# Optimization experiments

Measured on AMD Instinct MI355X. Metric: run time of the kernel, lower is better.

The kernel has to match this reference:

```python
import jax, jax.numpy as jnp
import numpy as np

B, T, D, H = 2, 2048, 768, 12
HS = D // H           # head_size = 64
FF = 4 * D            # feed_forward_multiplier = 4 -> hidden 3072
HALF = FF // 2        # SwiGLU halves hidden -> 1536
EPS = 1e-8


def rmsnorm(x, scale):
    # RMSNorm with p=-1: full-dim L2 norm / sqrt(d), then x/(rms+eps)*scale
    d = x.shape[-1]
    rms = jnp.linalg.norm(x, axis=-1, keepdims=True) * (d ** -0.5)
    return scale * (x / (rms + EPS))


def setup_inputs() -> dict:
    key = jax.random.key(0)
    ks = jax.random.split(key, 12)
    s = 0.02
    return {
        "x":  jax.random.normal(ks[0], (B, T, D), dtype=jnp.float32),
        "Wq": jax.random.normal(ks[1], (H, D, HS), dtype=jnp.float32) * s,
        "Wk": jax.random.normal(ks[2], (H, D, HS), dtype=jnp.float32) * s,
        "Wv": jax.random.normal(ks[3], (H, D, HS), dtype=jnp.float32) * s,
        "Wo": jax.random.normal(ks[4], (D, D), dtype=jnp.float32) * s,
        "bo": jnp.zeros((D,), dtype=jnp.float32),
        "W1": jax.random.normal(ks[5], (D, FF), dtype=jnp.float32) * s,
        "b1": jnp.zeros((FF,), dtype=jnp.float32),
        "W2": jax.random.normal(ks[6], (HALF, D), dtype=jnp.float32) * s,
        "b2": jnp.zeros((D,), dtype=jnp.float32),
        "g1": jnp.ones((D,), dtype=jnp.float32),
        "g2": jnp.ones((D,), dtype=jnp.float32),
    }


def reference(x, Wq, Wk, Wv, Wo, bo, W1, b1, W2, b2, g1, g2):
    Bx, Tx, Dx = x.shape
    # --- Multi-head causal attention (pre-RMSNorm, residual) ---
    h = rmsnorm(x, g1)
    q = jnp.einsum('btd,hdk->bhtk', h, Wq)
    k = jnp.einsum('btd,hdk->bhtk', h, Wk)
    v = jnp.einsum('btd,hdk->bhtk', h, Wv)
    # NOTE: original scales by C**-0.5 where C = embed_dim (not head_size)
    scores = jnp.einsum('bhtk,bhsk->bhts', q, k) * (Dx ** -0.5)
    causal = jnp.tril(jnp.ones((Tx, Tx), dtype=bool))
    scores = jnp.where(causal, scores, -jnp.inf)
    wei = jax.nn.softmax(scores, axis=-1)
    attn = jnp.einsum('bhts,bhsk->bhtk', wei, v)
    attn = attn.transpose(0, 2, 1, 3).reshape(Bx, Tx, Dx)  # concat heads
    x = x + attn @ Wo + bo
    # --- SwiGLU FFN (pre-RMSNorm, residual) ---
    h2 = rmsnorm(x, g2)
    u = h2 @ W1 + b1
    a, gate = jnp.split(u, 2, axis=-1)  # chunk: first half = value, second = gate
    x = x + (jax.nn.silu(gate) * a) @ W2 + b2
    return x
```

## Files before the change

### kernel.cpp

```cpp
#include <hip/hip_runtime.h>
#include <math.h>

#define TDIM 2048
#define DDIM 768
#define NH   12
#define NROWS 4096
#define EPSV 1e-8f
#define SCALE 0.03608439182435161f

typedef __bf16 bf16_t;
typedef bf16_t bf16x8 __attribute__((ext_vector_type(8)));
typedef bf16_t bf16x4 __attribute__((ext_vector_type(4)));
typedef bf16_t bf16x2 __attribute__((ext_vector_type(2)));
typedef float  floatx4 __attribute__((ext_vector_type(4)));

__device__ __forceinline__ void glds16(const bf16_t* g, bf16_t* l) {
    __builtin_amdgcn_global_load_lds(
        (const __attribute__((address_space(1))) void*)g,
        (__attribute__((address_space(3))) void*)l, 16, 0, 0);
}

__global__ __launch_bounds__(256) void pack_all(
    const float* __restrict__ Wq, const float* __restrict__ Wk,
    const float* __restrict__ Wv, const float* __restrict__ Wo,
    const float* __restrict__ W1, const float* __restrict__ W2,
    bf16_t* __restrict__ qkvw, bf16_t* __restrict__ wo,
    bf16_t* __restrict__ w1, bf16_t* __restrict__ w2)
{
    int bid = blockIdx.x;
    const float* src; bf16_t* dst;
    int srcld, dstld, k0, n0;
    int remap = 0;
    if (bid < 144) {
        int kx = bid % 12, nx = bid / 12;
        src = Wo; dst = wo; srcld = 768; dstld = 768; k0 = kx * 64; n0 = nx * 64;
    } else if (bid < 720) {
        int t = bid - 144; int kx = t % 12, nx = t / 12;
        src = W1; dst = w1; srcld = 3072; dstld = 768; k0 = kx * 64; n0 = nx * 64;
        remap = 1;
    } else if (bid < 1008) {
        int t = bid - 720; int kx = t % 24, nx = t / 24;
        src = W2; dst = w2; srcld = 768; dstld = 1536; k0 = kx * 64; n0 = nx * 64;
    } else {
        int t = bid - 1008; int kx = t % 12, y = t / 12;
        int sel = y / 12, h = y - sel * 12;
        src = ((sel == 0) ? Wq : (sel == 1) ? Wk : Wv) + (size_t)h * 768 * 64;
        dst = qkvw + (size_t)(sel * 768 + h * 64) * 768;
        srcld = 64; dstld = 768; k0 = kx * 64; n0 = 0;
    }
    __shared__ float Ts[64][65];
    int tid = threadIdx.x;
    int r = tid >> 2, c = (tid & 3) * 16;
    const float* s = src + (size_t)(k0 + r) * srcld + n0 + c;
    #pragma unroll
    for (int i = 0; i < 4; i++) {
        float4 t = *(const float4*)(s + i * 4);
        Ts[r][c + i*4 + 0] = t.x; Ts[r][c + i*4 + 1] = t.y;
        Ts[r][c + i*4 + 2] = t.z; Ts[r][c + i*4 + 3] = t.w;
    }
    __syncthreads();
    int n = tid >> 2, kk = (tid & 3) * 16;
    bf16x8 o0, o1;
    #pragma unroll
    for (int i = 0; i < 8; i++) {
        o0[i] = (bf16_t)Ts[kk + i][n];
        o1[i] = (bf16_t)Ts[kk + 8 + i][n];
    }
    int oc = n0 + n;
    if (remap) oc = (oc < 1536) ? (oc * 2) : ((oc - 1536) * 2 + 1);
    bf16_t* d = dst + (size_t)oc * dstld + k0 + kk;
    *(bf16x8*)d = o0;
    *(bf16x8*)(d + 8) = o1;
}

__global__ __launch_bounds__(256) void rmsnorm_bf(
    const float* __restrict__ x, const float* __restrict__ g,
    bf16_t* __restrict__ out)
{
    int row = blockIdx.x;
    int tid = threadIdx.x;
    const float* xr = x + (size_t)row * DDIM;
    float v0 = xr[tid], v1 = xr[tid + 256], v2 = xr[tid + 512];
    float s = v0*v0 + v1*v1 + v2*v2;
    #pragma unroll
    for (int off = 32; off > 0; off >>= 1)
        s += __shfl_down(s, off, 64);
    __shared__ float red[4];
    __shared__ float tot;
    if ((tid & 63) == 0) red[tid >> 6] = s;
    __syncthreads();
    if (tid == 0) tot = red[0] + red[1] + red[2] + red[3];
    __syncthreads();
    float rms = sqrtf(tot * (1.0f / DDIM));
    float inv = 1.0f / (rms + EPSV);
    bf16_t* orow = out + (size_t)row * DDIM;
    orow[tid]       = (bf16_t)(g[tid]       * v0 * inv);
    orow[tid + 256] = (bf16_t)(g[tid + 256] * v1 * inv);
    orow[tid + 512] = (bf16_t)(g[tid + 512] * v2 * inv);
}

template<int TM, int EPI>
__global__ __launch_bounds__(256) void gemm_bf16(
    const bf16_t* __restrict__ A, const bf16_t* __restrict__ BT, int K,
    float* __restrict__ Cf, bf16_t* __restrict__ Cb, int ldc,
    const float* __restrict__ bias, const float* __restrict__ resid)
{
    constexpr int MT = TM / 32;
    __shared__ bf16_t As0[TM][32], As1[TM][32];
    __shared__ bf16_t Bs0[128][32], Bs1[128][32];
    int tid = threadIdx.x;
    int wave = tid >> 6, lane = tid & 63;
    int lrow = lane & 15, quad = lane >> 4;
    int wm = wave >> 1, wn = wave & 1;

    int m0 = blockIdx.y * TM;
    int n0 = blockIdx.x * 128;

    int srow = lane >> 2, scol = (lane & 3) * 8;
    const bf16_t* Ag = A  + ((size_t)m0 + wave * (TM/4) + srow) * K + scol;
    const bf16_t* Bg = BT + ((size_t)n0 + wave * 32 + srow) * K + scol;

    floatx4 acc[MT][4];
    #pragma unroll
    for (int mt = 0; mt < MT; mt++)
        #pragma unroll
        for (int nt = 0; nt < 4; nt++)
            #pragma unroll
            for (int r = 0; r < 4; r++) acc[mt][nt][r] = 0.f;

    for (int k0 = 0; k0 < K; k0 += 64) {
        __syncthreads();
        #pragma unroll
        for (int i = 0; i < TM/64; i++) {
            glds16(Ag + (size_t)(i*16) * K + k0,      &As0[wave*(TM/4) + i*16][0]);
            glds16(Ag + (size_t)(i*16) * K + k0 + 32, &As1[wave*(TM/4) + i*16][0]);
        }
        #pragma unroll
        for (int i = 0; i < 2; i++) {
            glds16(Bg + (size_t)(i*16) * K + k0,      &Bs0[wave*32 + i*16][0]);
            glds16(Bg + (size_t)(i*16) * K + k0 + 32, &Bs1[wave*32 + i*16][0]);
        }
        __syncthreads();

        bf16x8 af0[MT], af1[MT], bf0[4], bf1[4];
        #pragma unroll
        for (int mt = 0; mt < MT; mt++) {
            af0[mt] = *(const bf16x8*)&As0[wm*(TM/2) + mt*16 + lrow][quad * 8];
            af1[mt] = *(const bf16x8*)&As1[wm*(TM/2) + mt*16 + lrow][quad * 8];
        }
        #pragma unroll
        for (int nt = 0; nt < 4; nt++) {
            bf0[nt] = *(const bf16x8*)&Bs0[wn*64 + nt*16 + lrow][quad * 8];
            bf1[nt] = *(const bf16x8*)&Bs1[wn*64 + nt*16 + lrow][quad * 8];
        }
        #pragma unroll
        for (int mt = 0; mt < MT; mt++)
            #pragma unroll
            for (int nt = 0; nt < 4; nt++) {
                acc[mt][nt] = __builtin_amdgcn_mfma_f32_16x16x32_bf16(
                    bf0[nt], af0[mt], acc[mt][nt], 0, 0, 0);
                acc[mt][nt] = __builtin_amdgcn_mfma_f32_16x16x32_bf16(
                    bf1[nt], af1[mt], acc[mt][nt], 0, 0, 0);
            }
    }

    int crow0 = m0 + wm * (TM/2);
    int ccol0 = n0 + wn * 64;
    #pragma unroll
    for (int mt = 0; mt < MT; mt++) {
        int row = crow0 + mt * 16 + lrow;
        #pragma unroll
        for (int nt = 0; nt < 4; nt++) {
            int col = ccol0 + nt * 16 + quad * 4;
            floatx4 a = acc[mt][nt];
            if constexpr (EPI == 1) {
                int c = col >> 1;
                float2 ba = *(const float2*)(bias + c);
                float2 bg = *(const float2*)(bias + 1536 + c);
                float a0 = a[0] + ba.x, g0 = a[1] + bg.x;
                float a1 = a[2] + ba.y, g1 = a[3] + bg.y;
                bf16x2 v;
                v[0] = (bf16_t)(a0 * (g0 / (1.0f + __expf(-g0))));
                v[1] = (bf16_t)(a1 * (g1 / (1.0f + __expf(-g1))));
                *(bf16x2*)(Cb + (size_t)row * ldc + c) = v;
            } else {
                size_t off = (size_t)row * ldc + col;
                float4 bv = make_float4(0.f, 0.f, 0.f, 0.f);
                if (bias) bv = *(const float4*)(bias + col);
                float4 rs = make_float4(0.f, 0.f, 0.f, 0.f);
                if (resid) rs = *(const float4*)(resid + off);
                if (Cf) {
                    float4 v;
                    v.x = a[0] + bv.x + rs.x; v.y = a[1] + bv.y + rs.y;
                    v.z = a[2] + bv.z + rs.z; v.w = a[3] + bv.w + rs.w;
                    *(float4*)(Cf + off) = v;
                } else {
                    bf16x4 v;
                    v[0] = (bf16_t)(a[0] + bv.x + rs.x);
                    v[1] = (bf16_t)(a[1] + bv.y + rs.y);
                    v[2] = (bf16_t)(a[2] + bv.z + rs.z);
                    v[3] = (bf16_t)(a[3] + bv.w + rs.w);
                    *(bf16x4*)(Cb + off) = v;
                }
            }
        }
    }
}

__global__ __launch_bounds__(256) void vt_kernel(
    const bf16_t* __restrict__ qkv, bf16_t* __restrict__ vt)
{
    __shared__ bf16_t Ts[64][72];
    int t0 = blockIdx.x * 64;
    int bh = blockIdx.y;
    int b = bh / NH, h = bh - b * NH;
    int tid = threadIdx.x;
    int r = tid >> 2, c = (tid & 3) * 16;
    const bf16_t* src = qkv + ((size_t)b * TDIM + t0 + r) * 2304 + 1536 + h * 64 + c;
    *(bf16x8*)&Ts[r][c]     = *(const bf16x8*)src;
    *(bf16x8*)&Ts[r][c + 8] = *(const bf16x8*)(src + 8);
    __syncthreads();
    int d = tid >> 2, tt = (tid & 3) * 16;
    bf16x8 o0, o1;
    #pragma unroll
    for (int i = 0; i < 8; i++) {
        o0[i] = Ts[tt + i][d];
        o1[i] = Ts[tt + 8 + i][d];
    }
    bf16_t* dst = vt + ((size_t)bh * 64 + d) * TDIM + t0 + tt;
    *(bf16x8*)dst = o0;
    *(bf16x8*)(dst + 8) = o1;
}

__global__ __launch_bounds__(256) void attn_mfma(
    const bf16_t* __restrict__ qkv, const bf16_t* __restrict__ vt,
    bf16_t* __restrict__ o)
{
    const int QS = 2304;
    int bid = blockIdx.x;
    int c = bid & 255, slot = bid >> 8;
    int x = c & 31, g = c >> 5;
    int qt, bh;
    if (slot == 0)      { bh = g;      qt = x; }
    else if (slot == 1) { bh = 8 + g;  qt = (x + 16) & 31; }
    else                { bh = 16 + g; qt = (x < 16) ? (31 - 2 * x) : (62 - 2 * x); }
    int b = bh / NH, h = bh - b * NH;
    int tid = threadIdx.x;
    int wave = tid >> 6, lane = tid & 63;
    int lrow = lane & 15, quad = lane >> 4;

    __shared__ bf16_t Ks[2][64][72];
    __shared__ bf16_t Vts[2][64][72];
    __shared__ bf16_t Ps[4][16][72];

    size_t rbase = (size_t)b * TDIM;
    int q0 = qt * 64, qrow_w = q0 + wave * 16;

    const bf16_t* qp = qkv + (rbase + qrow_w + lrow) * QS + h * 64;
    bf16x8 qf[2];
    qf[0] = *(const bf16x8*)(qp + quad * 8);
    qf[1] = *(const bf16x8*)(qp + 32 + quad * 8);

    floatx4 o_acc[4];
    #pragma unroll
    for (int mt = 0; mt < 4; mt++)
        #pragma unroll
        for (int r = 0; r < 4; r++) o_acc[mt][r] = 0.f;
    float m_r = -INFINITY, l_r = 0.f;

    int srow = tid >> 2;
    int scol = (tid & 3) * 16;
    const bf16_t* kbase = qkv + (rbase + srow) * QS + 768 + h * 64 + scol;
    const bf16_t* vbase = vt + ((size_t)bh * 64 + srow) * TDIM + scol;

    bf16x8 kr0 = *(const bf16x8*)kbase;
    bf16x8 kr1 = *(const bf16x8*)(kbase + 8);
    bf16x8 vr0 = *(const bf16x8*)vbase;
    bf16x8 vr1 = *(const bf16x8*)(vbase + 8);
    *(bf16x8*)&Ks[0][srow][scol]      = kr0;
    *(bf16x8*)&Ks[0][srow][scol + 8]  = kr1;
    *(bf16x8*)&Vts[0][srow][scol]     = vr0;
    *(bf16x8*)&Vts[0][srow][scol + 8] = vr1;
    if (qt >= 1) {
        const bf16_t* kp = kbase + (size_t)64 * QS;
        const bf16_t* vp = vbase + 64;
        kr0 = *(const bf16x8*)kp;  kr1 = *(const bf16x8*)(kp + 8);
        vr0 = *(const bf16x8*)vp;  vr1 = *(const bf16x8*)(vp + 8);
    }
    asm volatile("s_waitcnt lgkmcnt(0)" ::: "memory");
    __builtin_amdgcn_s_barrier();

    for (int s = 0; s <= qt; s++) {
        int cur = s & 1;

        floatx4 sfrag[4];
        __builtin_amdgcn_s_setprio(1);
        #pragma unroll
        for (int nt = 0; nt < 4; nt++) {
            floatx4 a;
            #pragma unroll
            for (int r = 0; r < 4; r++) a[r] = 0.f;
            #pragma unroll
            for (int kf = 0; kf < 2; kf++) {
                bf16x8 afr = *(const bf16x8*)&Ks[cur][nt * 16 + lrow][kf * 32 + quad * 8];
                a = __builtin_amdgcn_mfma_f32_16x16x32_bf16(afr, qf[kf], a, 0, 0, 0);
            }
            sfrag[nt] = a;
        }
        __builtin_amdgcn_s_setprio(0);

        if (s == qt) {
            int qg = qrow_w + lrow;
            #pragma unroll
            for (int nt = 0; nt < 4; nt++)
                #pragma unroll
                for (int r = 0; r < 4; r++) {
                    int kc = s * 64 + nt * 16 + quad * 4 + r;
                    sfrag[nt][r] = (kc > qg) ? -INFINITY : sfrag[nt][r] * SCALE;
                }
        } else {
            #pragma unroll
            for (int nt = 0; nt < 4; nt++)
                #pragma unroll
                for (int r = 0; r < 4; r++) sfrag[nt][r] *= SCALE;
        }

        float mx = sfrag[0][0];
        #pragma unroll
        for (int nt = 0; nt < 4; nt++)
            #pragma unroll
            for (int r = 0; r < 4; r++) mx = fmaxf(mx, sfrag[nt][r]);
        mx = fmaxf(mx, __shfl_xor(mx, 16, 64));
        mx = fmaxf(mx, __shfl_xor(mx, 32, 64));
        if (__any(mx > m_r + 8.0f)) {
            float mn = fmaxf(m_r, mx);
            float alpha = __expf(m_r - mn);
            m_r = mn;
            l_r *= alpha;
            #pragma unroll
            for (int mt = 0; mt < 4; mt++)
                #pragma unroll
                for (int r = 0; r < 4; r++) o_acc[mt][r] *= alpha;
        }

        float ls = 0.f;
        #pragma unroll
        for (int nt = 0; nt < 4; nt++) {
            bf16x4 pv;
            #pragma unroll
            for (int r = 0; r < 4; r++) {
                float p = __expf(sfrag[nt][r] - m_r);
                ls += p;
                pv[r] = (bf16_t)p;
            }
            *(bf16x4*)&Ps[wave][lrow][nt * 16 + quad * 4] = pv;
        }
        ls += __shfl_xor(ls, 16, 64);
        ls += __shfl_xor(ls, 32, 64);
        l_r += ls;

        __builtin_amdgcn_s_setprio(1);
        #pragma unroll
        for (int kf = 0; kf < 2; kf++) {
            bf16x8 pfr = *(const bf16x8*)&Ps[wave][lrow][kf * 32 + quad * 8];
            #pragma unroll
            for (int mt = 0; mt < 4; mt++) {
                bf16x8 vfr = *(const bf16x8*)&Vts[cur][mt * 16 + lrow][kf * 32 + quad * 8];
                o_acc[mt] = __builtin_amdgcn_mfma_f32_16x16x32_bf16(vfr, pfr, o_acc[mt], 0, 0, 0);
            }
        }
        __builtin_amdgcn_s_setprio(0);

        if (s < qt) {
            int nxt = cur ^ 1;
            *(bf16x8*)&Ks[nxt][srow][scol]      = kr0;
            *(bf16x8*)&Ks[nxt][srow][scol + 8]  = kr1;
            *(bf16x8*)&Vts[nxt][srow][scol]     = vr0;
            *(bf16x8*)&Vts[nxt][srow][scol + 8] = vr1;
        }

        if (s + 2 <= qt) {
            const bf16_t* kp = kbase + (size_t)(s + 2) * 64 * QS;
            const bf16_t* vp = vbase + (size_t)(s + 2) * 64;
            kr0 = *(const bf16x8*)kp;  kr1 = *(const bf16x8*)(kp + 8);
            vr0 = *(const bf16x8*)vp;  vr1 = *(const bf16x8*)(vp + 8);
        }

        asm volatile("s_waitcnt lgkmcnt(0)" ::: "memory");
        __builtin_amdgcn_s_barrier();
    }

    float inv = 1.0f / l_r;
    size_t rb = (rbase + qrow_w + lrow) * DDIM + h * 64;
    #pragma unroll
    for (int mt = 0; mt < 4; mt++) {
        bf16x4 ov;
        #pragma unroll
        for (int r = 0; r < 4; r++) ov[r] = (bf16_t)(o_acc[mt][r] * inv);
        *(bf16x4*)(o + rb + mt * 16 + quad * 4) = ov;
    }
}

extern "C" void kernel_launch(void* const* d_in, const int* in_sizes, int n_in,
                              void* d_out, int out_size, void* d_ws, size_t ws_size,
                              hipStream_t stream) {
    const float* x  = (const float*)d_in[0];
    const float* Wq = (const float*)d_in[1];
    const float* Wk = (const float*)d_in[2];
    const float* Wv = (const float*)d_in[3];
    const float* Wo = (const float*)d_in[4];
    const float* bo = (const float*)d_in[5];
    const float* W1 = (const float*)d_in[6];
    const float* b1 = (const float*)d_in[7];
    const float* W2 = (const float*)d_in[8];
    const float* b2 = (const float*)d_in[9];
    const float* g1 = (const float*)d_in[10];
    const float* g2 = (const float*)d_in[11];
    float* out = (float*)d_out;
    char* ws = (char*)d_ws;

    bf16_t* qkvw_bt = (bf16_t*)(ws);
    bf16_t* wo_bt   = (bf16_t*)(ws + 3538944);
    bf16_t* w1_bt   = (bf16_t*)(ws + 4718592);
    bf16_t* w2_bt   = (bf16_t*)(ws + 9437184);
    bf16_t* h_bf    = (bf16_t*)(ws + 11796480);
    bf16_t* qkv     = (bf16_t*)(ws + 18087936);
    bf16_t* attn_bf = (bf16_t*)(ws + 36962304);
    bf16_t* sw_bf   = (bf16_t*)(ws + 68419584);
    bf16_t* vt      = (bf16_t*)(ws + 81002496);

    pack_all<<<1440, 256, 0, stream>>>(Wq, Wk, Wv, Wo, W1, W2,
                                       qkvw_bt, wo_bt, w1_bt, w2_bt);

    rmsnorm_bf<<<NROWS, 256, 0, stream>>>(x, g1, h_bf);

    gemm_bf16<128, 0><<<dim3(18, 32), 256, 0, stream>>>(
        h_bf, qkvw_bt, 768, nullptr, qkv, 2304, nullptr, nullptr);

    vt_kernel<<<dim3(32, 24), 256, 0, stream>>>(qkv, vt);

    attn_mfma<<<768, 256, 0, stream>>>(qkv, vt, attn_bf);

    gemm_bf16<64, 0><<<dim3(6, 64), 256, 0, stream>>>(
        attn_bf, wo_bt, 768, out, nullptr, 768, bo, x);

    rmsnorm_bf<<<NROWS, 256, 0, stream>>>(out, g2, h_bf);

    gemm_bf16<128, 1><<<dim3(24, 32), 256, 0, stream>>>(
        h_bf, w1_bt, 768, nullptr, sw_bf, 1536, b1, nullptr);

    gemm_bf16<64, 0><<<dim3(6, 64), 256, 0, stream>>>(
        sw_bf, w2_bt, 1536, out, nullptr, 768, b2, out);
}
```

Before: 265.4 us.

## Split attention KV loop across two wave groups with final softmax merge

The attention kernel now launches 512 threads per block. Two groups of four waves each handle alternating KV tiles, each group keeping its own online-softmax state. At the end the partial outputs and max/sum statistics are merged through shared memory. This halves the serial KV-loop length per block and raises parallelism for the causal attention, at the cost of extra block-wide barriers, a merge step, larger register pressure under launch bounds of 512, and more shared memory per block.

```diff
diff --git a/kernel.cpp b/kernel.cpp
--- a/kernel.cpp
+++ b/kernel.cpp
@@ -232,29 +232,33 @@
     *(bf16x8*)(dst + 8) = o1;
 }
 
-__global__ __launch_bounds__(256) void attn_mfma(
+__global__ __launch_bounds__(512) void attn_mfma(
     const bf16_t* __restrict__ qkv, const bf16_t* __restrict__ vt,
     bf16_t* __restrict__ o)
 {
     const int QS = 2304;
     int bid = blockIdx.x;
     int c = bid & 255, slot = bid >> 8;
-    int x = c & 31, g = c >> 5;
+    int x = c & 31, gg = c >> 5;
     int qt, bh;
-    if (slot == 0)      { bh = g;      qt = x; }
-    else if (slot == 1) { bh = 8 + g;  qt = (x + 16) & 31; }
-    else                { bh = 16 + g; qt = (x < 16) ? (31 - 2 * x) : (62 - 2 * x); }
+    if (slot == 0)      { bh = gg;      qt = x; }
+    else if (slot == 1) { bh = 8 + gg;  qt = (x + 16) & 31; }
+    else                { bh = 16 + gg; qt = (x < 16) ? (31 - 2 * x) : (62 - 2 * x); }
     int b = bh / NH, h = bh - b * NH;
     int tid = threadIdx.x;
     int wave = tid >> 6, lane = tid & 63;
+    int ww = wave & 3;
+    int g  = wave >> 2;
     int lrow = lane & 15, quad = lane >> 4;
 
     __shared__ bf16_t Ks[2][64][72];
     __shared__ bf16_t Vts[2][64][72];
-    __shared__ bf16_t Ps[4][16][72];
+    __shared__ char ps_raw[8 * 16 * 72 * 2];
+    __shared__ float Ml[4][16][2];
+    bf16_t (*Ps)[16][72] = (bf16_t (*)[16][72])ps_raw;
 
     size_t rbase = (size_t)b * TDIM;
-    int q0 = qt * 64, qrow_w = q0 + wave * 16;
+    int q0 = qt * 64, qrow_w = q0 + ww * 16;
 
     const bf16_t* qp = qkv + (rbase + qrow_w + lrow) * QS + h * 64;
     bf16x8 qf[2];
@@ -268,136 +272,161 @@
         for (int r = 0; r < 4; r++) o_acc[mt][r] = 0.f;
     float m_r = -INFINITY, l_r = 0.f;
 
-    int srow = tid >> 2;
-    int scol = (tid & 3) * 16;
+    int st = tid & 255;
+    int srow = st >> 2;
+    int scol = (st & 3) * 16;
     const bf16_t* kbase = qkv + (rbase + srow) * QS + 768 + h * 64 + scol;
     const bf16_t* vbase = vt + ((size_t)bh * 64 + srow) * TDIM + scol;
 
-    bf16x8 kr0 = *(const bf16x8*)kbase;
-    bf16x8 kr1 = *(const bf16x8*)(kbase + 8);
-    bf16x8 vr0 = *(const bf16x8*)vbase;
-    bf16x8 vr1 = *(const bf16x8*)(vbase + 8);
-    *(bf16x8*)&Ks[0][srow][scol]      = kr0;
-    *(bf16x8*)&Ks[0][srow][scol + 8]  = kr1;
-    *(bf16x8*)&Vts[0][srow][scol]     = vr0;
-    *(bf16x8*)&Vts[0][srow][scol + 8] = vr1;
-    if (qt >= 1) {
-        const bf16_t* kp = kbase + (size_t)64 * QS;
-        const bf16_t* vp = vbase + 64;
+    bf16x8 kr0, kr1, vr0, vr1;
+    if (g <= qt) {
+        const bf16_t* kp = kbase + (size_t)g * 64 * QS;
+        const bf16_t* vp = vbase + (size_t)g * 64;
         kr0 = *(const bf16x8*)kp;  kr1 = *(const bf16x8*)(kp + 8);
         vr0 = *(const bf16x8*)vp;  vr1 = *(const bf16x8*)(vp + 8);
+        *(bf16x8*)&Ks[g][srow][scol]      = kr0;
+        *(bf16x8*)&Ks[g][srow][scol + 8]  = kr1;
+        *(bf16x8*)&Vts[g][srow][scol]     = vr0;
+        *(bf16x8*)&Vts[g][srow][scol + 8] = vr1;
+    }
+    if (g + 2 <= qt) {
+        const bf16_t* kp = kbase + (size_t)(g + 2) * 64 * QS;
+        const bf16_t* vp = vbase + (size_t)(g + 2) * 64;
+        kr0 = *(const bf16x8*)kp;  kr1 = *(const bf16x8*)(kp + 8);
+        vr0 = *(const bf16x8*)vp;  vr1 = *(const bf16x8*)(vp + 8);
     }
     asm volatile("s_waitcnt lgkmcnt(0)" ::: "memory");
     __builtin_amdgcn_s_barrier();
 
-    for (int s = 0; s <= qt; s++) {
-        int cur = s & 1;
-
-        floatx4 sfrag[4];
-        __builtin_amdgcn_s_setprio(1);
-        #pragma unroll
-        for (int nt = 0; nt < 4; nt++) {
-            floatx4 a;
-            #pragma unroll
-            for (int r = 0; r < 4; r++) a[r] = 0.f;
+    int nit = (qt >> 1) + 1;
+    for (int i = 0; i < nit; i++) {
+        int s = 2 * i + g;
+        if (s <= qt) {
+            floatx4 sfrag[4];
+            __builtin_amdgcn_s_setprio(1);
+            #pragma unroll
+            for (int nt = 0; nt < 4; nt++) {
+                floatx4 a;
+                #pragma unroll
+                for (int r = 0; r < 4; r++) a[r] = 0.f;
+                #pragma unroll
+                for (int kf = 0; kf < 2; kf++) {
+                    bf16x8 afr = *(const bf16x8*)&Ks[g][nt * 16 + lrow][kf * 32 + quad * 8];
+                    a = __builtin_amdgcn_mfma_f32_16x16x32_bf16(afr, qf[kf], a, 0, 0, 0);
+                }
+                sfrag[nt] = a;
+            }
+            __builtin_amdgcn_s_setprio(0);
+
+            if (s == qt) {
+                int qg = qrow_w + lrow;
+                #pragma unroll
+                for (int nt = 0; nt < 4; nt++)
+                    #pragma unroll
+                    for (int r = 0; r < 4; r++) {
+                        int kc = s * 64 + nt * 16 + quad * 4 + r;
+                        sfrag[nt][r] = (kc > qg) ? -INFINITY : sfrag[nt][r] * SCALE;
+                    }
+            } else {
+                #pragma unroll
+                for (int nt = 0; nt < 4; nt++)
+                    #pragma unroll
+                    for (int r = 0; r < 4; r++) sfrag[nt][r] *= SCALE;
+            }
+
+            float mx = sfrag[0][0];
+            #pragma unroll
+            for (int nt = 0; nt < 4; nt++)
+                #pragma unroll
+                for (int r = 0; r < 4; r++) mx = fmaxf(mx, sfrag[nt][r]);
+            mx = fmaxf(mx, __shfl_xor(mx, 16, 64));
+            mx = fmaxf(mx, __shfl_xor(mx, 32, 64));
+            if (__any(mx > m_r + 8.0f)) {
+                float mn = fmaxf(m_r, mx);
+                float alpha = __expf(m_r - mn);
+                m_r = mn;
+                l_r *= alpha;
+                #pragma unroll
+                for (int mt = 0; mt < 4; mt++)
+                    #pragma unroll
+                    for (int r = 0; r < 4; r++) o_acc[mt][r] *= alpha;
+            }
+
+            float ls = 0.f;
+            #pragma unroll
+            for (int nt = 0; nt < 4; nt++) {
+                bf16x4 pv;
+                #pragma unroll
+                for (int r = 0; r < 4; r++) {
+                    float p = __expf(sfrag[nt][r] - m_r);
+                    ls += p;
+                    pv[r] = (bf16_t)p;
+                }
+                *(bf16x4*)&Ps[wave][lrow][nt * 16 + quad * 4] = pv;
+            }
+            ls += __shfl_xor(ls, 16, 64);
+            ls += __shfl_xor(ls, 32, 64);
+            l_r += ls;
+
+            __builtin_amdgcn_s_setprio(1);
             #pragma unroll
             for (int kf = 0; kf < 2; kf++) {
-                bf16x8 afr = *(const bf16x8*)&Ks[cur][nt * 16 + lrow][kf * 32 + quad * 8];
-                a = __builtin_amdgcn_mfma_f32_16x16x32_bf16(afr, qf[kf], a, 0, 0, 0);
-            }
-            sfrag[nt] = a;
-        }
-        __builtin_amdgcn_s_setprio(0);
-
-        if (s == qt) {
-            int qg = qrow_w + lrow;
-            #pragma unroll
-            for (int nt = 0; nt < 4; nt++)
-                #pragma unroll
-                for (int r = 0; r < 4; r++) {
-                    int kc = s * 64 + nt * 16 + quad * 4 + r;
-                    sfrag[nt][r] = (kc > qg) ? -INFINITY : sfrag[nt][r] * SCALE;
+                bf16x8 pfr = *(const bf16x8*)&Ps[wave][lrow][kf * 32 + quad * 8];
+                #pragma unroll
+                for (int mt = 0; mt < 4; mt++) {
+                    bf16x8 vfr = *(const bf16x8*)&Vts[g][mt * 16 + lrow][kf * 32 + quad * 8];
+                    o_acc[mt] = __builtin_amdgcn_mfma_f32_16x16x32_bf16(vfr, pfr, o_acc[mt], 0, 0, 0);
                 }
-        } else {
-            #pragma unroll
-            for (int nt = 0; nt < 4; nt++)
-                #pragma unroll
-                for (int r = 0; r < 4; r++) sfrag[nt][r] *= SCALE;
-        }
-
-        float mx = sfrag[0][0];
-        #pragma unroll
-        for (int nt = 0; nt < 4; nt++)
-            #pragma unroll
-            for (int r = 0; r < 4; r++) mx = fmaxf(mx, sfrag[nt][r]);
-        mx = fmaxf(mx, __shfl_xor(mx, 16, 64));
-        mx = fmaxf(mx, __shfl_xor(mx, 32, 64));
-        if (__any(mx > m_r + 8.0f)) {
-            float mn = fmaxf(m_r, mx);
-            float alpha = __expf(m_r - mn);
-            m_r = mn;
-            l_r *= alpha;
-            #pragma unroll
-            for (int mt = 0; mt < 4; mt++)
-                #pragma unroll
-                for (int r = 0; r < 4; r++) o_acc[mt][r] *= alpha;
-        }
-
-        float ls = 0.f;
-        #pragma unroll
-        for (int nt = 0; nt < 4; nt++) {
-            bf16x4 pv;
-            #pragma unroll
-            for (int r = 0; r < 4; r++) {
-                float p = __expf(sfrag[nt][r] - m_r);
-                ls += p;
-                pv[r] = (bf16_t)p;
-            }
-            *(bf16x4*)&Ps[wave][lrow][nt * 16 + quad * 4] = pv;
-        }
-        ls += __shfl_xor(ls, 16, 64);
-        ls += __shfl_xor(ls, 32, 64);
-        l_r += ls;
-
-        __builtin_amdgcn_s_setprio(1);
-        #pragma unroll
-        for (int kf = 0; kf < 2; kf++) {
-            bf16x8 pfr = *(const bf16x8*)&Ps[wave][lrow][kf * 32 + quad * 8];
-            #pragma unroll
-            for (int mt = 0; mt < 4; mt++) {
-                bf16x8 vfr = *(const bf16x8*)&Vts[cur][mt * 16 + lrow][kf * 32 + quad * 8];
-                o_acc[mt] = __builtin_amdgcn_mfma_f32_16x16x32_bf16(vfr, pfr, o_acc[mt], 0, 0, 0);
-            }
-        }
-        __builtin_amdgcn_s_setprio(0);
-
-        if (s < qt) {
-            int nxt = cur ^ 1;
-            *(bf16x8*)&Ks[nxt][srow][scol]      = kr0;
-            *(bf16x8*)&Ks[nxt][srow][scol + 8]  = kr1;
-            *(bf16x8*)&Vts[nxt][srow][scol]     = vr0;
-            *(bf16x8*)&Vts[nxt][srow][scol + 8] = vr1;
-        }
-
-        if (s + 2 <= qt) {
-            const bf16_t* kp = kbase + (size_t)(s + 2) * 64 * QS;
-            const bf16_t* vp = vbase + (size_t)(s + 2) * 64;
+            }
+            __builtin_amdgcn_s_setprio(0);
+        }
+
+        __syncthreads();
+
+        if (2 * (i + 1) + g <= qt) {
+            *(bf16x8*)&Ks[g][srow][scol]      = kr0;
+            *(bf16x8*)&Ks[g][srow][scol + 8]  = kr1;
+            *(bf16x8*)&Vts[g][srow][scol]     = vr0;
+            *(bf16x8*)&Vts[g][srow][scol + 8] = vr1;
+        }
+        if (2 * (i + 2) + g <= qt) {
+            const bf16_t* kp = kbase + (size_t)(2 * (i + 2) + g) * 64 * QS;
+            const bf16_t* vp = vbase + (size_t)(2 * (i + 2) + g) * 64;
             kr0 = *(const bf16x8*)kp;  kr1 = *(const bf16x8*)(kp + 8);
             vr0 = *(const bf16x8*)vp;  vr1 = *(const bf16x8*)(vp + 8);
         }
-
         asm volatile("s_waitcnt lgkmcnt(0)" ::: "memory");
         __builtin_amdgcn_s_barrier();
     }
 
-    float inv = 1.0f / l_r;
-    size_t rb = (rbase + qrow_w + lrow) * DDIM + h * 64;
-    #pragma unroll
-    for (int mt = 0; mt < 4; mt++) {
-        bf16x4 ov;
-        #pragma unroll
-        for (int r = 0; r < 4; r++) ov[r] = (bf16_t)(o_acc[mt][r] * inv);
-        *(bf16x4*)(o + rb + mt * 16 + quad * 4) = ov;
+    float* Om = (float*)ps_raw;
+    if (g == 1) {
+        float* orow = Om + ((size_t)ww * 16 + lrow) * 72;
+        #pragma unroll
+        for (int mt = 0; mt < 4; mt++)
+            *(float4*)(orow + mt * 16 + quad * 4) =
+                make_float4(o_acc[mt][0], o_acc[mt][1], o_acc[mt][2], o_acc[mt][3]);
+        if (quad == 0) { Ml[ww][lrow][0] = m_r; Ml[ww][lrow][1] = l_r; }
+    }
+    __syncthreads();
+    if (g == 0) {
+        float m1 = Ml[ww][lrow][0], l1 = Ml[ww][lrow][1];
+        float M = fmaxf(m_r, m1);
+        float a0 = __expf(m_r - M);
+        float a1 = (m1 == -INFINITY) ? 0.f : __expf(m1 - M);
+        float linv = 1.0f / (a0 * l_r + a1 * l1);
+        const float* orow = Om + ((size_t)ww * 16 + lrow) * 72;
+        size_t rb = (rbase + qrow_w + lrow) * DDIM + h * 64;
+        #pragma unroll
+        for (int mt = 0; mt < 4; mt++) {
+            float4 p = *(const float4*)(orow + mt * 16 + quad * 4);
+            bf16x4 ov;
+            ov[0] = (bf16_t)((a0 * o_acc[mt][0] + a1 * p.x) * linv);
+            ov[1] = (bf16_t)((a0 * o_acc[mt][1] + a1 * p.y) * linv);
+            ov[2] = (bf16_t)((a0 * o_acc[mt][2] + a1 * p.z) * linv);
+            ov[3] = (bf16_t)((a0 * o_acc[mt][3] + a1 * p.w) * linv);
+            *(bf16x4*)(o + rb + mt * 16 + quad * 4) = ov;
+        }
     }
 }
 
@@ -439,7 +468,7 @@
 
     vt_kernel<<<dim3(32, 24), 256, 0, stream>>>(qkv, vt);
 
-    attn_mfma<<<768, 256, 0, stream>>>(qkv, vt, attn_bf);
+    attn_mfma<<<768, 512, 0, stream>>>(qkv, vt, attn_bf);
 
     gemm_bf16<64, 0><<<dim3(6, 64), 256, 0, stream>>>(
         attn_bf, wo_bt, 768, out, nullptr, 768, bo, x);
```

Measured after the change: 266.6 us. No clear change (+0.5%).
